# Performance work log

Hardware: AMD Instinct MI355X
Metric: run time of the kernel (lower is better)

The kernel has to match this reference:

```python
import jax, jax.numpy as jnp
import numpy as np

SDF_W = 7000.0
EIK_W = 600.0
ORI_W = 500.0
NEAR_ORI_W = 10.0
GRADN_W = 200.0
K_NEIGHBORS = 2


def _orientation_sign(query, surface, normals, k=K_NEIGHBORS):
    # Original detaches to numpy for a scipy KDTree query -> stop_gradient here.
    q = jax.lax.stop_gradient(query)       # [Q,3]
    s = jax.lax.stop_gradient(surface)     # [S,3]
    n = jax.lax.stop_gradient(normals)     # [S,3]
    # Brute-force squared distances [Q,S] (GEMM-dominated).
    d2 = (jnp.sum(q * q, axis=-1, keepdims=True)
          - 2.0 * (q @ s.T)
          + jnp.sum(s * s, axis=-1)[None, :])
    _, idx = jax.lax.top_k(-d2, k)         # [Q,k] nearest-neighbor indices
    near_pts = s[idx]                      # [Q,k,3]
    near_nrm = n[idx]                      # [Q,k,3]
    vecs = q[:, None, :] - near_pts        # [Q,k,3]
    dots = jnp.sum(vecs * near_nrm, axis=-1)  # [Q,k]
    return jnp.sign(jnp.mean(dots, axis=1))   # [Q]


def setup_inputs() -> dict:
    key = jax.random.key(0)
    ks = jax.random.split(key, 8)
    N = 16384
    return {
        "manifold_pred": jax.random.normal(ks[0], (N, 1), jnp.float32) * 0.1,
        "manifold_grad": jax.random.normal(ks[1], (N, 3), jnp.float32),
        "nonmanifold_pred": jax.random.normal(ks[2], (N, 1), jnp.float32),
        "near_points_pred": jax.random.normal(ks[3], (N, 1), jnp.float32) * 0.1,
        "surface_points": jax.random.normal(ks[4], (N, 3), jnp.float32),
        "surface_normals": jax.random.normal(ks[5], (N, 3), jnp.float32),
        "off_surface_points": jax.random.normal(ks[6], (N, 3), jnp.float32) * 1.5,
        "near_points": jax.random.normal(ks[7], (N, 3), jnp.float32),
    }


def reference(manifold_pred, manifold_grad, nonmanifold_pred, near_points_pred,
              surface_points, surface_normals, off_surface_points, near_points):
    sdf_loss = jnp.mean(manifold_pred ** 2)
    eikonal_loss = jnp.mean((jnp.linalg.norm(manifold_grad, axis=-1) - 1.0) ** 2)

    signs_off = _orientation_sign(off_surface_points, surface_points, surface_normals)
    orientation_loss = jnp.mean(jax.nn.relu(-nonmanifold_pred * signs_off[:, None]))

    signs_near = _orientation_sign(near_points, surface_points, surface_normals)
    near_surface_orientation_loss = jnp.mean(jax.nn.relu(-near_points_pred * signs_near[:, None]))

    gradient_normal_loss = jnp.mean((manifold_grad - surface_normals) ** 2)

    total = (SDF_W * sdf_loss + EIK_W * eikonal_loss + ORI_W * orientation_loss
             + NEAR_ORI_W * near_surface_orientation_loss + GRADN_W * gradient_normal_loss)
    return (total, sdf_loss, eikonal_loss, orientation_loss,
            near_surface_orientation_loss, gradient_normal_loss)
```

## Files before the change

### kernel.cpp

```cpp
#include <hip/hip_runtime.h>
#include <math.h>

#define SDF_W      7000.0f
#define EIK_W      600.0f
#define ORI_W      500.0f
#define NEAR_ORI_W 10.0f
#define GRADN_W    200.0f

#define TILE   2048
#define NWAVE  8
#define CHK    64
#define QPL    8
#define QB     (QPL * 64)
#define NSPLIT 8
#define QPW    8
#define WS_STRIDE 8192
#define WS_REC 65536


__device__ __forceinline__ float neg_half_norm2(float sx, float sy, float sz) {
    return -0.5f * fmaf(sx, sx, fmaf(sy, sy, sz * sz));
}
__device__ __forceinline__ float score(float qx, float qy, float qz,
                                       float sx, float sy, float sz, float nh) {
    return fmaf(qx, sx, fmaf(qy, sy, fmaf(qz, sz, nh)));
}

__device__ __forceinline__ float dot_at(const float* __restrict__ surf,
                                        const float* __restrict__ norms, int j,
                                        float qx, float qy, float qz) {
    float sx = surf[3*j], sy = surf[3*j+1], sz = surf[3*j+2];
    float nx = norms[3*j], ny = norms[3*j+1], nz = norms[3*j+2];
    return fmaf(qx - sx, nx, fmaf(qy - sy, ny, (qz - sz) * nz));
}

__global__ __launch_bounds__(512, 4) void nn_scan(
    const float* __restrict__ offq, const float* __restrict__ nearq,
    const float* __restrict__ surf,
    float* __restrict__ ws, int S, int Qoff, int QT)
{
    __shared__ float4 tile[TILE];
    const int t    = threadIdx.x;
    const int lane = t & 63;
    const int wv   = __builtin_amdgcn_readfirstlane(t >> 6);

    const int qgroup = blockIdx.x >> 3;
    const int part   = blockIdx.x & 7;

    const int partLen = (((S + NSPLIT - 1) / NSPLIT) + (CHK - 1)) & ~(CHK - 1);
    int sb = part * partLen;       if (sb > S) sb = S;
    int se = sb + partLen;         if (se > S) se = S;

    const int qbase = qgroup * QB;
    float qx[QPL], qy[QPL], qz[QPL];
    #pragma unroll
    for (int j = 0; j < QPL; ++j) {
        int q = qbase + j * 64 + lane;
        qx[j] = 0.f; qy[j] = 0.f; qz[j] = 0.f;
        if (q < QT) {
            const float* p = (q < Qoff) ? (offq + 3 * q) : (nearq + 3 * (q - Qoff));
            qx[j] = p[0]; qy[j] = p[1]; qz[j] = p[2];
        }
    }

    float M1[QPL], M2[QPL], P1[QPL], P2[QPL];
    int c1[QPL], c2[QPL];
    #pragma unroll
    for (int j = 0; j < QPL; ++j) {
        M1[j] = -3.0e38f; M2[j] = -3.0e38f;
        P1[j] = -3.0e38f; P2[j] = -3.0e38f;
        c1[j] = 0; c2[j] = 0;
    }

    for (int base = sb; base < se; base += TILE) {
        __syncthreads();
        {
            int p0 = base + t * 4;
            if (p0 + 4 <= se) {
                const float4* g4 = (const float4*)(surf + 3 * p0);
                float4 r0 = g4[0], r1 = g4[1], r2 = g4[2];
                tile[t*4+0] = make_float4(r0.x, r0.y, r0.z, neg_half_norm2(r0.x, r0.y, r0.z));
                tile[t*4+1] = make_float4(r0.w, r1.x, r1.y, neg_half_norm2(r0.w, r1.x, r1.y));
                tile[t*4+2] = make_float4(r1.z, r1.w, r2.x, neg_half_norm2(r1.z, r1.w, r2.x));
                tile[t*4+3] = make_float4(r2.y, r2.z, r2.w, neg_half_norm2(r2.y, r2.z, r2.w));
            } else {
                #pragma unroll
                for (int k = 0; k < 4; ++k) {
                    int p = p0 + k;
                    if (p < se) {
                        float sx = surf[3*p], sy = surf[3*p+1], sz = surf[3*p+2];
                        tile[t*4+k] = make_float4(sx, sy, sz, neg_half_norm2(sx, sy, sz));
                    } else {
                        tile[t*4+k] = make_float4(0.f, 0.f, 0.f, -3.0e38f);
                    }
                }
            }
        }
        __syncthreads();
        const int lo = wv * (TILE / NWAVE);
        const float4* tp = tile + lo;
        const int ccbase = (base + lo) >> 6;
        #pragma unroll 1
        for (int c4 = 0; c4 < (TILE / NWAVE) / CHK; ++c4) {
            const float4* cp = tp + c4 * CHK;
            #pragma unroll 2
            for (int o = 0; o < CHK; ++o) {
                float4 s4 = cp[o];
                #pragma unroll
                for (int j = 0; j < QPL; ++j) {
                    float g = score(qx[j], qy[j], qz[j], s4.x, s4.y, s4.z, s4.w);
                    M2[j] = __builtin_amdgcn_fmed3f(g, M1[j], M2[j]);
                    M1[j] = fmaxf(M1[j], g);
                }
            }
            int cid = ccbase + c4;
            #pragma unroll
            for (int j = 0; j < QPL; ++j) {
                c1[j] = (M1[j] != P1[j]) ? cid : c1[j];  P1[j] = M1[j];
                c2[j] = (M2[j] != P2[j]) ? cid : c2[j];  P2[j] = M2[j];
            }
        }
    }

    __syncthreads();
    float4* rec = tile;
    if (wv < 4) {
        #pragma unroll
        for (int j = 0; j < QPL; ++j)
            rec[wv * QB + j * 64 + lane] =
                make_float4(M1[j], M2[j], __int_as_float(c1[j]), __int_as_float(c2[j]));
    }
    __syncthreads();
    float m1 = -3.0e38f, m2 = -3.0e38f;
    int k1 = 0, k2 = 0;
    #pragma unroll
    for (int w = 0; w < 4; ++w) {
        float4 a = rec[w * QB + t];
        float a1 = a.x, a2 = a.y;
        int ac1 = __float_as_int(a.z), ac2 = __float_as_int(a.w);
        if (a1 > m1)      { m2 = m1; k2 = k1; m1 = a1; k1 = ac1; }
        else if (a1 > m2) { m2 = a1; k2 = ac1; }
        if (a2 > m2)      { m2 = a2; k2 = ac2; }
    }
    __syncthreads();
    if (wv >= 4) {
        #pragma unroll
        for (int j = 0; j < QPL; ++j)
            rec[(wv - 4) * QB + j * 64 + lane] =
                make_float4(M1[j], M2[j], __int_as_float(c1[j]), __int_as_float(c2[j]));
    }
    __syncthreads();
    #pragma unroll
    for (int w = 0; w < 4; ++w) {
        float4 a = rec[w * QB + t];
        float a1 = a.x, a2 = a.y;
        int ac1 = __float_as_int(a.z), ac2 = __float_as_int(a.w);
        if (a1 > m1)      { m2 = m1; k2 = k1; m1 = a1; k1 = ac1; }
        else if (a1 > m2) { m2 = a1; k2 = ac1; }
        if (a2 > m2)      { m2 = a2; k2 = ac2; }
    }
    int gq = qbase + t;
    if (gq < QT) {
        ((float4*)(ws + WS_REC))[gq * NSPLIT + part] =
            make_float4(m1, m2, __int_as_float(k1), __int_as_float(k2));
    }
}

__global__ __launch_bounds__(512) void recover_k(
    const float* __restrict__ offq, const float* __restrict__ nearq,
    const float* __restrict__ surf, const float* __restrict__ norms,
    const float* __restrict__ nmpred, const float* __restrict__ nppred,
    const float* __restrict__ mp, const float* __restrict__ mg,
    const float* __restrict__ sn,
    float* __restrict__ ws, int S, int Qoff, int QT, int N)
{
    const int t    = threadIdx.x;
    const int lane = t & 63;
    const int wv   = t >> 6;

    float accOri = 0.f, accNori = 0.f;
    const int q0 = (blockIdx.x * NWAVE + wv) * QPW;
    const float4* recs = (const float4*)(ws + WS_REC);

    for (int u = 0; u < QPW; ++u) {
        int q = q0 + u;
        if (q >= QT) break;

        float M1 = -3.0e38f, M2 = -3.0e38f;
        int c1 = 0, c2 = 0;
        #pragma unroll
        for (int h = 0; h < NSPLIT; ++h) {
            float4 r = recs[q * NSPLIT + h];
            float a1 = r.x, a2 = r.y;
            int ac1 = __float_as_int(r.z), ac2 = __float_as_int(r.w);
            if (a1 > M1)      { M2 = M1; c2 = c1; M1 = a1; c1 = ac1; }
            else if (a1 > M2) { M2 = a1; c2 = ac1; }
            if (a2 > M2)      { M2 = a2; c2 = ac2; }
        }
        bool isNear = (q >= Qoff);
        const float* qp = isNear ? (nearq + 3 * (q - Qoff)) : (offq + 3 * q);
        float qx = qp[0], qy = qp[1], qz = qp[2];

        int j1 = c1 * CHK + lane;
        int j2 = c2 * CHK + lane;
        float g1 = -3.0e38f, dot1 = 0.f, g2 = -3.0e38f, dot2 = 0.f;
        if (j1 < S) {
            float sx = surf[3*j1], sy = surf[3*j1+1], sz = surf[3*j1+2];
            float nx = norms[3*j1], ny = norms[3*j1+1], nz = norms[3*j1+2];
            g1 = score(qx, qy, qz, sx, sy, sz, neg_half_norm2(sx, sy, sz));
            dot1 = fmaf(qx - sx, nx, fmaf(qy - sy, ny, (qz - sz) * nz));
        }
        if (j2 < S) {
            float sx = surf[3*j2], sy = surf[3*j2+1], sz = surf[3*j2+2];
            float nx = norms[3*j2], ny = norms[3*j2+1], nz = norms[3*j2+2];
            g2 = score(qx, qy, qz, sx, sy, sz, neg_half_norm2(sx, sy, sz));
            dot2 = fmaf(qx - sx, nx, fmaf(qy - sy, ny, (qz - sz) * nz));
        }

        unsigned long long m1mask = __ballot(g1 == M1);
        int I1; float d1;
        if (m1mask) {
            int l1 = __ffsll(m1mask) - 1;
            I1 = c1 * CHK + l1;
            d1 = __shfl(dot1, l1);
        } else {
            I1 = 0;
            d1 = dot_at(surf, norms, 0, qx, qy, qz);
        }

        unsigned long long m2mask = __ballot(g2 == M2);
        int rel = I1 - c2 * CHK;
        if (rel >= 0 && rel < 64) m2mask &= ~(1ull << rel);
        float d2;
        if (m2mask) {
            int l2 = __ffsll(m2mask) - 1;
            d2 = __shfl(dot2, l2);
        } else {
            int I2 = (I1 == 0 && S > 1) ? 1 : 0;
            d2 = dot_at(surf, norms, I2, qx, qy, qz);
        }

        float ms = d1 + d2;
        float sgn = (ms > 0.f) ? 1.f : ((ms < 0.f) ? -1.f : 0.f);
        float pred = isNear ? nppred[q - Qoff] : nmpred[q];
        float term = fmaxf(0.f, -pred * sgn);
        if (lane == 0) {
            if (isNear) accNori += term; else accOri += term;
        }
    }

    float sdf = 0.f, eik = 0.f, gn = 0.f;
    for (int i = blockIdx.x * 512 + t; i < N; i += gridDim.x * 512) {
        float p = mp[i];
        sdf += p * p;
        float gx = mg[3*i], gy = mg[3*i+1], gz = mg[3*i+2];
        float nrm = sqrtf(fmaf(gx, gx, fmaf(gy, gy, gz * gz)));
        float d = nrm - 1.0f;
        eik += d * d;
        float nx = sn[3*i], ny = sn[3*i+1], nz = sn[3*i+2];
        float dx = gx - nx, dy = gy - ny, dz = gz - nz;
        gn += fmaf(dx, dx, fmaf(dy, dy, dz * dz));
    }

    float v0 = accOri, v1 = accNori, v2 = sdf, v3 = eik, v4 = gn;
    #pragma unroll
    for (int off = 32; off > 0; off >>= 1) {
        v0 += __shfl_down(v0, off);
        v1 += __shfl_down(v1, off);
        v2 += __shfl_down(v2, off);
        v3 += __shfl_down(v3, off);
        v4 += __shfl_down(v4, off);
    }
    __shared__ float red[5][NWAVE];
    if (lane == 0) {
        red[0][wv] = v0; red[1][wv] = v1; red[2][wv] = v2;
        red[3][wv] = v3; red[4][wv] = v4;
    }
    __syncthreads();
    if (t == 0) {
        #pragma unroll
        for (int k = 0; k < 5; ++k) {
            float s = 0.f;
            #pragma unroll
            for (int w = 0; w < NWAVE; ++w) s += red[k][w];
            ws[k * WS_STRIDE + blockIdx.x] = s;
        }
    }
}

__global__ __launch_bounds__(256) void final_k(
    const float* __restrict__ ws, float* __restrict__ out,
    int N, int RB, int Qoff, int Qnear)
{
    __shared__ float r[5][256];
    int t = threadIdx.x;
    float s[5] = {0.f, 0.f, 0.f, 0.f, 0.f};
    for (int i = t; i < RB; i += 256) {
        #pragma unroll
        for (int k = 0; k < 5; ++k) s[k] += ws[k * WS_STRIDE + i];
    }
    #pragma unroll
    for (int k = 0; k < 5; ++k) r[k][t] = s[k];
    __syncthreads();
    for (int off = 128; off > 0; off >>= 1) {
        if (t < off) {
            #pragma unroll
            for (int k = 0; k < 5; ++k) r[k][t] += r[k][t + off];
        }
        __syncthreads();
    }
    if (t == 0) {
        float orim  = r[0][0] / (float)Qoff;
        float norim = r[1][0] / (float)Qnear;
        float sdfm  = r[2][0] / (float)N;
        float eikm  = r[3][0] / (float)N;
        float gnm   = r[4][0] / (3.0f * (float)N);
        out[0] = SDF_W * sdfm + EIK_W * eikm + ORI_W * orim
               + NEAR_ORI_W * norim + GRADN_W * gnm;
        out[1] = sdfm;
        out[2] = eikm;
        out[3] = orim;
        out[4] = norim;
        out[5] = gnm;
    }
}

extern "C" void kernel_launch(void* const* d_in, const int* in_sizes, int n_in,
                              void* d_out, int out_size, void* d_ws, size_t ws_size,
                              hipStream_t stream)
{
    const float* mp    = (const float*)d_in[0];
    const float* mg    = (const float*)d_in[1];
    const float* nmp   = (const float*)d_in[2];
    const float* npp   = (const float*)d_in[3];
    const float* sp    = (const float*)d_in[4];
    const float* sn    = (const float*)d_in[5];
    const float* offp  = (const float*)d_in[6];
    const float* nearp = (const float*)d_in[7];
    float* out = (float*)d_out;

    const int N     = in_sizes[0];
    const int S     = in_sizes[4] / 3;
    const int Qoff  = in_sizes[2];
    const int Qnear = in_sizes[3];
    const int QT    = Qoff + Qnear;

    float* ws = (float*)d_ws;

    const int qgroups = (QT + QB - 1) / QB;
    const int RBLK    = (QT + NWAVE * QPW - 1) / (NWAVE * QPW);

    nn_scan<<<qgroups * NSPLIT, 512, 0, stream>>>(offp, nearp, sp, ws, S, Qoff, QT);
    recover_k<<<RBLK, 512, 0, stream>>>(offp, nearp, sp, sn, nmp, npp,
                                        mp, mg, sn, ws, S, Qoff, QT, N);
    final_k<<<1, 256, 0, stream>>>(ws, out, N, RBLK, Qoff, Qnear);
}
```

Before: 166.3 us.

## Restructure NN scan: per-wave query batches, lane-strided surface reads, prepacked float4 surface

A new pre-pass packs the surface points into float4 records that carry the negative half squared norm. The NN scan now assigns 16 queries per wave, with the queries held uniformly across lanes. Each lane streams its own strided subset of surface points directly from global memory and prefetches the next one, which replaces the LDS tiling and the 8-way split of the surface set. The per-query top-2 is merged across lanes with shuffles, so the cross-block partial records and the merge step in recover_k go away. This trades LDS reuse for global/L2 reads and adds one extra launch; the lower occupancy target (waves_per_eu 2) frees registers for the larger query batch.

```diff
diff --git a/kernel.cpp b/kernel.cpp
--- a/kernel.cpp
+++ b/kernel.cpp
@@ -7,15 +7,10 @@
 #define NEAR_ORI_W 10.0f
 #define GRADN_W    200.0f
 
-#define TILE   2048
 #define NWAVE  8
-#define CHK    64
-#define QPL    8
-#define QB     (QPL * 64)
-#define NSPLIT 8
+#define QW     16
+#define CHKI   32
 #define QPW    8
-#define WS_STRIDE 8192
-#define WS_REC 65536
 
 
 __device__ __forceinline__ float neg_half_norm2(float sx, float sy, float sz) {
@@ -26,218 +21,167 @@
     return fmaf(qx, sx, fmaf(qy, sy, fmaf(qz, sz, nh)));
 }
 
-__device__ __forceinline__ float dot_at(const float* __restrict__ surf,
-                                        const float* __restrict__ norms, int j,
-                                        float qx, float qy, float qz) {
-    float sx = surf[3*j], sy = surf[3*j+1], sz = surf[3*j+2];
-    float nx = norms[3*j], ny = norms[3*j+1], nz = norms[3*j+2];
-    return fmaf(qx - sx, nx, fmaf(qy - sy, ny, (qz - sz) * nz));
-}
-
-__global__ __launch_bounds__(512, 4) void nn_scan(
-    const float* __restrict__ offq, const float* __restrict__ nearq,
-    const float* __restrict__ surf,
-    float* __restrict__ ws, int S, int Qoff, int QT)
-{
-    __shared__ float4 tile[TILE];
-    const int t    = threadIdx.x;
-    const int lane = t & 63;
-    const int wv   = __builtin_amdgcn_readfirstlane(t >> 6);
-
-    const int qgroup = blockIdx.x >> 3;
-    const int part   = blockIdx.x & 7;
-
-    const int partLen = (((S + NSPLIT - 1) / NSPLIT) + (CHK - 1)) & ~(CHK - 1);
-    int sb = part * partLen;       if (sb > S) sb = S;
-    int se = sb + partLen;         if (se > S) se = S;
-
-    const int qbase = qgroup * QB;
-    float qx[QPL], qy[QPL], qz[QPL];
+__device__ __forceinline__ float dot_fmt(const float4* __restrict__ fmt,
+                                         const float* __restrict__ norms, int j,
+                                         float qx, float qy, float qz) {
+    float4 s = fmt[j];
+    return fmaf(qx - s.x, norms[3*j],
+           fmaf(qy - s.y, norms[3*j+1], (qz - s.z) * norms[3*j+2]));
+}
+
+__global__ __launch_bounds__(256) void fmt_k(
+    const float* __restrict__ surf, float4* __restrict__ fmt, int S, int SPfull)
+{
+    int p = blockIdx.x * 256 + threadIdx.x;
+    if (p >= SPfull) return;
+    if (p < S) {
+        float sx = surf[3*p], sy = surf[3*p+1], sz = surf[3*p+2];
+        fmt[p] = make_float4(sx, sy, sz, neg_half_norm2(sx, sy, sz));
+    } else {
+        fmt[p] = make_float4(0.f, 0.f, 0.f, -3.0e38f);
+    }
+}
+
+__global__ __launch_bounds__(512) __attribute__((amdgpu_waves_per_eu(2, 2)))
+void nn_scan(const float* __restrict__ offq, const float* __restrict__ nearq,
+             const float4* __restrict__ fmt, float4* __restrict__ recs,
+             int nIter, int Qoff, int QT)
+{
+    const int lane = threadIdx.x & 63;
+    const int wv   = __builtin_amdgcn_readfirstlane((int)threadIdx.x >> 6);
+    const int qbase = (blockIdx.x * NWAVE + wv) * QW;
+
+    float qx[QW], qy[QW], qz[QW];
     #pragma unroll
-    for (int j = 0; j < QPL; ++j) {
-        int q = qbase + j * 64 + lane;
-        qx[j] = 0.f; qy[j] = 0.f; qz[j] = 0.f;
+    for (int j = 0; j < QW; ++j) {
+        int q = qbase + j;
+        float x = 0.f, y = 0.f, z = 0.f;
         if (q < QT) {
             const float* p = (q < Qoff) ? (offq + 3 * q) : (nearq + 3 * (q - Qoff));
-            qx[j] = p[0]; qy[j] = p[1]; qz[j] = p[2];
-        }
-    }
-
-    float M1[QPL], M2[QPL], P1[QPL], P2[QPL];
-    int c1[QPL], c2[QPL];
+            x = p[0]; y = p[1]; z = p[2];
+        }
+        qx[j] = x; qy[j] = y; qz[j] = z;
+    }
+
+    float M1[QW], M2[QW];
+    int id1[QW], id2[QW];
     #pragma unroll
-    for (int j = 0; j < QPL; ++j) {
-        M1[j] = -3.0e38f; M2[j] = -3.0e38f;
-        P1[j] = -3.0e38f; P2[j] = -3.0e38f;
-        c1[j] = 0; c2[j] = 0;
-    }
-
-    for (int base = sb; base < se; base += TILE) {
-        __syncthreads();
-        {
-            int p0 = base + t * 4;
-            if (p0 + 4 <= se) {
-                const float4* g4 = (const float4*)(surf + 3 * p0);
-                float4 r0 = g4[0], r1 = g4[1], r2 = g4[2];
-                tile[t*4+0] = make_float4(r0.x, r0.y, r0.z, neg_half_norm2(r0.x, r0.y, r0.z));
-                tile[t*4+1] = make_float4(r0.w, r1.x, r1.y, neg_half_norm2(r0.w, r1.x, r1.y));
-                tile[t*4+2] = make_float4(r1.z, r1.w, r2.x, neg_half_norm2(r1.z, r1.w, r2.x));
-                tile[t*4+3] = make_float4(r2.y, r2.z, r2.w, neg_half_norm2(r2.y, r2.z, r2.w));
+    for (int j = 0; j < QW; ++j) {
+        M1[j] = -3.0e38f; M2[j] = -3.0e38f; id1[j] = 0; id2[j] = 0;
+    }
+
+    const int nCh = (nIter + CHKI - 1) / CHKI;
+    const float4* fp = fmt + lane;
+    float4 cur = fp[0];
+    int i = 0;
+    #pragma unroll 1
+    for (int cc = 0; cc < nCh; ++cc) {
+        float P1[QW], P2[QW];
+        #pragma unroll
+        for (int j = 0; j < QW; ++j) { P1[j] = M1[j]; P2[j] = M2[j]; }
+        const int iEnd = min(nIter, (cc + 1) * CHKI);
+        #pragma unroll 2
+        for (; i < iEnd; ++i) {
+            float4 nxt = fp[(i + 1) * 64];
+            #pragma unroll
+            for (int j = 0; j < QW; ++j) {
+                float g = score(qx[j], qy[j], qz[j], cur.x, cur.y, cur.z, cur.w);
+                M2[j] = __builtin_amdgcn_fmed3f(g, M1[j], M2[j]);
+                M1[j] = fmaxf(M1[j], g);
+            }
+            cur = nxt;
+        }
+        const int cid = (cc << 6) | lane;
+        #pragma unroll
+        for (int j = 0; j < QW; ++j) {
+            id1[j] = (M1[j] != P1[j]) ? cid : id1[j];
+            id2[j] = (M2[j] != P2[j]) ? cid : id2[j];
+        }
+    }
+
+    #pragma unroll 1
+    for (int j = 0; j < QW; ++j) {
+        float m1 = M1[j], m2 = M2[j];
+        int i1 = id1[j], i2 = id2[j];
+        #pragma unroll
+        for (int off = 32; off > 0; off >>= 1) {
+            float b1 = __shfl_down(m1, off);
+            float b2 = __shfl_down(m2, off);
+            int   c1 = __shfl_down(i1, off);
+            int   c2 = __shfl_down(i2, off);
+            if (b1 > m1) {
+                bool ka = (m1 > b2);
+                m2 = ka ? m1 : b2;  i2 = ka ? i1 : c2;
+                m1 = b1;            i1 = c1;
             } else {
-                #pragma unroll
-                for (int k = 0; k < 4; ++k) {
-                    int p = p0 + k;
-                    if (p < se) {
-                        float sx = surf[3*p], sy = surf[3*p+1], sz = surf[3*p+2];
-                        tile[t*4+k] = make_float4(sx, sy, sz, neg_half_norm2(sx, sy, sz));
-                    } else {
-                        tile[t*4+k] = make_float4(0.f, 0.f, 0.f, -3.0e38f);
-                    }
-                }
+                bool kb = (b1 > m2);
+                m2 = kb ? b1 : m2;  i2 = kb ? c1 : i2;
             }
         }
-        __syncthreads();
-        const int lo = wv * (TILE / NWAVE);
-        const float4* tp = tile + lo;
-        const int ccbase = (base + lo) >> 6;
-        #pragma unroll 1
-        for (int c4 = 0; c4 < (TILE / NWAVE) / CHK; ++c4) {
-            const float4* cp = tp + c4 * CHK;
-            #pragma unroll 2
-            for (int o = 0; o < CHK; ++o) {
-                float4 s4 = cp[o];
-                #pragma unroll
-                for (int j = 0; j < QPL; ++j) {
-                    float g = score(qx[j], qy[j], qz[j], s4.x, s4.y, s4.z, s4.w);
-                    M2[j] = __builtin_amdgcn_fmed3f(g, M1[j], M2[j]);
-                    M1[j] = fmaxf(M1[j], g);
-                }
-            }
-            int cid = ccbase + c4;
-            #pragma unroll
-            for (int j = 0; j < QPL; ++j) {
-                c1[j] = (M1[j] != P1[j]) ? cid : c1[j];  P1[j] = M1[j];
-                c2[j] = (M2[j] != P2[j]) ? cid : c2[j];  P2[j] = M2[j];
-            }
-        }
-    }
-
-    __syncthreads();
-    float4* rec = tile;
-    if (wv < 4) {
-        #pragma unroll
-        for (int j = 0; j < QPL; ++j)
-            rec[wv * QB + j * 64 + lane] =
-                make_float4(M1[j], M2[j], __int_as_float(c1[j]), __int_as_float(c2[j]));
-    }
-    __syncthreads();
-    float m1 = -3.0e38f, m2 = -3.0e38f;
-    int k1 = 0, k2 = 0;
-    #pragma unroll
-    for (int w = 0; w < 4; ++w) {
-        float4 a = rec[w * QB + t];
-        float a1 = a.x, a2 = a.y;
-        int ac1 = __float_as_int(a.z), ac2 = __float_as_int(a.w);
-        if (a1 > m1)      { m2 = m1; k2 = k1; m1 = a1; k1 = ac1; }
-        else if (a1 > m2) { m2 = a1; k2 = ac1; }
-        if (a2 > m2)      { m2 = a2; k2 = ac2; }
-    }
-    __syncthreads();
-    if (wv >= 4) {
-        #pragma unroll
-        for (int j = 0; j < QPL; ++j)
-            rec[(wv - 4) * QB + j * 64 + lane] =
-                make_float4(M1[j], M2[j], __int_as_float(c1[j]), __int_as_float(c2[j]));
-    }
-    __syncthreads();
-    #pragma unroll
-    for (int w = 0; w < 4; ++w) {
-        float4 a = rec[w * QB + t];
-        float a1 = a.x, a2 = a.y;
-        int ac1 = __float_as_int(a.z), ac2 = __float_as_int(a.w);
-        if (a1 > m1)      { m2 = m1; k2 = k1; m1 = a1; k1 = ac1; }
-        else if (a1 > m2) { m2 = a1; k2 = ac1; }
-        if (a2 > m2)      { m2 = a2; k2 = ac2; }
-    }
-    int gq = qbase + t;
-    if (gq < QT) {
-        ((float4*)(ws + WS_REC))[gq * NSPLIT + part] =
-            make_float4(m1, m2, __int_as_float(k1), __int_as_float(k2));
-    }
-}
-
-__global__ __launch_bounds__(512) void recover_k(
-    const float* __restrict__ offq, const float* __restrict__ nearq,
-    const float* __restrict__ surf, const float* __restrict__ norms,
-    const float* __restrict__ nmpred, const float* __restrict__ nppred,
-    const float* __restrict__ mp, const float* __restrict__ mg,
-    const float* __restrict__ sn,
-    float* __restrict__ ws, int S, int Qoff, int QT, int N)
+        if (lane == 0 && qbase + j < QT)
+            recs[qbase + j] = make_float4(m1, m2, __int_as_float(i1), __int_as_float(i2));
+    }
+}
+
+__global__ __launch_bounds__(512) __attribute__((amdgpu_waves_per_eu(4, 4)))
+void recover_k(const float* __restrict__ offq, const float* __restrict__ nearq,
+               const float4* __restrict__ fmt, const float* __restrict__ norms,
+               const float* __restrict__ nmpred, const float* __restrict__ nppred,
+               const float* __restrict__ mp, const float* __restrict__ mg,
+               const float* __restrict__ sn,
+               const float4* __restrict__ recs, float* __restrict__ partials,
+               int S, int Qoff, int QT, int N, int RB)
 {
     const int t    = threadIdx.x;
     const int lane = t & 63;
     const int wv   = t >> 6;
+    const int q0   = (blockIdx.x * NWAVE + wv) * QPW;
 
     float accOri = 0.f, accNori = 0.f;
-    const int q0 = (blockIdx.x * NWAVE + wv) * QPW;
-    const float4* recs = (const float4*)(ws + WS_REC);
-
     for (int u = 0; u < QPW; ++u) {
         int q = q0 + u;
         if (q >= QT) break;
-
-        float M1 = -3.0e38f, M2 = -3.0e38f;
-        int c1 = 0, c2 = 0;
-        #pragma unroll
-        for (int h = 0; h < NSPLIT; ++h) {
-            float4 r = recs[q * NSPLIT + h];
-            float a1 = r.x, a2 = r.y;
-            int ac1 = __float_as_int(r.z), ac2 = __float_as_int(r.w);
-            if (a1 > M1)      { M2 = M1; c2 = c1; M1 = a1; c1 = ac1; }
-            else if (a1 > M2) { M2 = a1; c2 = ac1; }
-            if (a2 > M2)      { M2 = a2; c2 = ac2; }
-        }
+        float4 r = recs[q];
+        float M1 = r.x, M2 = r.y;
+        int i1 = __float_as_int(r.z), i2 = __float_as_int(r.w);
+        int cc1 = i1 >> 6, ln1 = i1 & 63;
+        int cc2 = i2 >> 6, ln2 = i2 & 63;
+
         bool isNear = (q >= Qoff);
         const float* qp = isNear ? (nearq + 3 * (q - Qoff)) : (offq + 3 * q);
         float qx = qp[0], qy = qp[1], qz = qp[2];
 
-        int j1 = c1 * CHK + lane;
-        int j2 = c2 * CHK + lane;
-        float g1 = -3.0e38f, dot1 = 0.f, g2 = -3.0e38f, dot2 = 0.f;
-        if (j1 < S) {
-            float sx = surf[3*j1], sy = surf[3*j1+1], sz = surf[3*j1+2];
-            float nx = norms[3*j1], ny = norms[3*j1+1], nz = norms[3*j1+2];
-            g1 = score(qx, qy, qz, sx, sy, sz, neg_half_norm2(sx, sy, sz));
-            dot1 = fmaf(qx - sx, nx, fmaf(qy - sy, ny, (qz - sz) * nz));
-        }
-        if (j2 < S) {
-            float sx = surf[3*j2], sy = surf[3*j2+1], sz = surf[3*j2+2];
-            float nx = norms[3*j2], ny = norms[3*j2+1], nz = norms[3*j2+2];
-            g2 = score(qx, qy, qz, sx, sy, sz, neg_half_norm2(sx, sy, sz));
-            dot2 = fmaf(qx - sx, nx, fmaf(qy - sy, ny, (qz - sz) * nz));
-        }
-
-        unsigned long long m1mask = __ballot(g1 == M1);
-        int I1; float d1;
-        if (m1mask) {
-            int l1 = __ffsll(m1mask) - 1;
-            I1 = c1 * CHK + l1;
-            d1 = __shfl(dot1, l1);
+        int half = lane >> 5;
+        int k    = lane & 31;
+        int p    = ((half ? cc2 : cc1) * CHKI + k) * 64 + (half ? ln2 : ln1);
+        float target = half ? M2 : M1;
+        float g = -3.0e38f, dotv = 0.f;
+        if (p < S) {
+            float4 s4 = fmt[p];
+            g = score(qx, qy, qz, s4.x, s4.y, s4.z, s4.w);
+            float nx = norms[3*p], ny = norms[3*p+1], nz = norms[3*p+2];
+            dotv = fmaf(qx - s4.x, nx, fmaf(qy - s4.y, ny, (qz - s4.z) * nz));
+        }
+        unsigned long long m = __ballot(g == target);
+        unsigned int lo = (unsigned int)m;
+        unsigned int hi = (unsigned int)(m >> 32);
+
+        float d1, d2;
+        int k1 = -1;
+        if (lo) {
+            k1 = __ffs(lo) - 1;
+            d1 = __shfl(dotv, k1);
         } else {
-            I1 = 0;
-            d1 = dot_at(surf, norms, 0, qx, qy, qz);
-        }
-
-        unsigned long long m2mask = __ballot(g2 == M2);
-        int rel = I1 - c2 * CHK;
-        if (rel >= 0 && rel < 64) m2mask &= ~(1ull << rel);
-        float d2;
-        if (m2mask) {
-            int l2 = __ffsll(m2mask) - 1;
-            d2 = __shfl(dot2, l2);
+            d1 = dot_fmt(fmt, norms, 0, qx, qy, qz);
+        }
+        if (M1 == M2 && i1 == i2 && k1 >= 0) hi &= ~(1u << k1);
+        if (hi) {
+            int k2 = __ffs(hi) - 1;
+            d2 = __shfl(dotv, 32 + k2);
         } else {
+            int I1 = (k1 >= 0) ? ((cc1 * CHKI + k1) * 64 + ln1) : 0;
             int I2 = (I1 == 0 && S > 1) ? 1 : 0;
-            d2 = dot_at(surf, norms, I2, qx, qy, qz);
+            d2 = dot_fmt(fmt, norms, I2, qx, qy, qz);
         }
 
         float ms = d1 + d2;
@@ -250,7 +194,7 @@
     }
 
     float sdf = 0.f, eik = 0.f, gn = 0.f;
-    for (int i = blockIdx.x * 512 + t; i < N; i += gridDim.x * 512) {
+    for (int i = blockIdx.x * 512 + t; i < N; i += (int)gridDim.x * 512) {
         float p = mp[i];
         sdf += p * p;
         float gx = mg[3*i], gy = mg[3*i+1], gz = mg[3*i+2];
@@ -279,17 +223,17 @@
     __syncthreads();
     if (t == 0) {
         #pragma unroll
-        for (int k = 0; k < 5; ++k) {
+        for (int kk = 0; kk < 5; ++kk) {
             float s = 0.f;
             #pragma unroll
-            for (int w = 0; w < NWAVE; ++w) s += red[k][w];
-            ws[k * WS_STRIDE + blockIdx.x] = s;
+            for (int w = 0; w < NWAVE; ++w) s += red[kk][w];
+            partials[kk * RB + blockIdx.x] = s;
         }
     }
 }
 
 __global__ __launch_bounds__(256) void final_k(
-    const float* __restrict__ ws, float* __restrict__ out,
+    const float* __restrict__ partials, float* __restrict__ out,
     int N, int RB, int Qoff, int Qnear)
 {
     __shared__ float r[5][256];
@@ -297,7 +241,7 @@
     float s[5] = {0.f, 0.f, 0.f, 0.f, 0.f};
     for (int i = t; i < RB; i += 256) {
         #pragma unroll
-        for (int k = 0; k < 5; ++k) s[k] += ws[k * WS_STRIDE + i];
+        for (int k = 0; k < 5; ++k) s[k] += partials[k * RB + i];
     }
     #pragma unroll
     for (int k = 0; k < 5; ++k) r[k][t] = s[k];
@@ -345,13 +289,20 @@
     const int Qnear = in_sizes[3];
     const int QT    = Qoff + Qnear;
 
-    float* ws = (float*)d_ws;
-
-    const int qgroups = (QT + QB - 1) / QB;
-    const int RBLK    = (QT + NWAVE * QPW - 1) / (NWAVE * QPW);
-
-    nn_scan<<<qgroups * NSPLIT, 512, 0, stream>>>(offp, nearp, sp, ws, S, Qoff, QT);
-    recover_k<<<RBLK, 512, 0, stream>>>(offp, nearp, sp, sn, nmp, npp,
-                                        mp, mg, sn, ws, S, Qoff, QT, N);
-    final_k<<<1, 256, 0, stream>>>(ws, out, N, RBLK, Qoff, Qnear);
-}
+    const int nIter  = (S + 63) / 64;
+    const int SPfull = nIter * 64 + 64;
+
+    float4* fmt      = (float4*)d_ws;
+    float4* recs     = fmt + SPfull;
+    float*  partials = (float*)(recs + QT);
+
+    const int RB         = (QT + NWAVE * QPW - 1) / (NWAVE * QPW);
+    const int scanBlocks = (QT + NWAVE * QW - 1) / (NWAVE * QW);
+
+    fmt_k<<<(SPfull + 255) / 256, 256, 0, stream>>>(sp, fmt, S, SPfull);
+    nn_scan<<<scanBlocks, 512, 0, stream>>>(offp, nearp, fmt, recs, nIter, Qoff, QT);
+    recover_k<<<RB, 512, 0, stream>>>(offp, nearp, fmt, sn, nmp, npp,
+                                      mp, mg, sn, recs, partials,
+                                      S, Qoff, QT, N, RB);
+    final_k<<<1, 256, 0, stream>>>(partials, out, N, RB, Qoff, Qnear);
+}
```

After: 179.0 us. 7.6% more time.
